# Kernel optimization log

Hardware: AMD Instinct MI355X
Metric: run time of the kernel (lower is better)

## Reference

```python
import jax, jax.numpy as jnp
import numpy as np


def haar_level(x):
    """One 2D Haar (periodization-equivalent for even sizes) DWT on [B,K,C,H,W].
    Returns [B,4K,C,H/2,W/2] with per-parent band order (LL, Hx, Hy, Hxy),
    matching the tree's append order yl, yh0, yh1, yh2."""
    B, K, C, H, W = x.shape
    x = x.reshape(B, K, C, H // 2, 2, W // 2, 2)
    a = x[:, :, :, :, 0, :, 0]
    b = x[:, :, :, :, 0, :, 1]
    c = x[:, :, :, :, 1, :, 0]
    d = x[:, :, :, :, 1, :, 1]
    ll = (a + b + c + d) * 0.5
    h1 = (a - b + c - d) * 0.5   # high along width
    h2 = (a + b - c - d) * 0.5   # high along height
    h3 = (a - b - c + d) * 0.5   # diagonal
    out = jnp.stack([ll, h1, h2, h3], axis=2)  # [B,K,4,C,H/2,W/2]
    return out.reshape(B, 4 * K, C, H // 2, W // 2)


def conv2d(x, w, b, stride, pad):
    y = jax.lax.conv_general_dilated(
        x, w, window_strides=(stride, stride),
        padding=[(pad, pad), (pad, pad)],
        dimension_numbers=('NCHW', 'OIHW', 'NCHW'))
    return y + b[None, :, None, None]


def setup_inputs() -> dict:
    key = jax.random.key(0)
    ks = jax.random.split(key, 9)
    s = 0.05
    return {
        'x':        jax.random.normal(ks[0], (64, 3, 224, 224), dtype=jnp.float32),
        'w_s1':     jax.random.normal(ks[1], (192, 3, 7, 7), dtype=jnp.float32) * s,
        'b_s1':     jax.random.normal(ks[2], (192,), dtype=jnp.float32) * s,
        'w_s2':     jax.random.normal(ks[3], (192, 192, 7, 7), dtype=jnp.float32) * s,
        'b_s2':     jax.random.normal(ks[4], (192,), dtype=jnp.float32) * s,
        'w_p':      jax.random.normal(ks[5], (768, 960, 3, 3), dtype=jnp.float32) * s,
        'b_p':      jax.random.normal(ks[6], (768,), dtype=jnp.float32) * s,
        'cls_token': jax.random.normal(ks[7], (1, 1, 768), dtype=jnp.float32),
        'positions': jax.random.normal(ks[8], (50, 768), dtype=jnp.float32),
    }


def reference(x, w_s1, b_s1, w_s2, b_s2, w_p, b_p, cls_token, positions):
    B = x.shape[0]
    # ---- 4-level full Haar wavelet packet tree (vectorized over subbands) ----
    t = x[:, None]                      # [B,1,3,224,224]
    for _ in range(4):
        t = haar_level(t)               # -> [B,256,3,14,14]
    wav = t.reshape(B, 256 * 3, 14, 14)  # [B,768,14,14] (tree concat order)
    # ---- spatial branch: two strided 7x7 convs (224 -> 56 -> 14) ----
    sp = conv2d(x, w_s1, b_s1, stride=4, pad=3)
    sp = conv2d(sp, w_s2, b_s2, stride=4, pad=3)   # [B,192,14,14]
    feat = jnp.concatenate([wav, sp], axis=1)      # [B,960,14,14]
    # ---- patch projection conv 3x3 s2 -> 7x7, flatten to tokens ----
    y = conv2d(feat, w_p, b_p, stride=2, pad=1)    # [B,768,7,7]
    y = y.reshape(B, 768, 49).transpose(0, 2, 1)   # [B,49,768]
    cls = jnp.broadcast_to(cls_token, (B, 1, 768))
    y = jnp.concatenate([cls, y], axis=1) + positions  # [B,50,768]
    return y
```

## Files before the change

### kernel.cpp

```cpp
#include <hip/hip_runtime.h>
#include <stdint.h>

typedef __attribute__((ext_vector_type(8))) short short8;
typedef __attribute__((ext_vector_type(4))) float floatx4;

__device__ inline unsigned short f2bf(float f){
  union { float fv; unsigned int u; } v; v.fv = f;
  unsigned int u = v.u;
  unsigned int r = ((u >> 16) & 1u) + 0x7FFFu;
  return (unsigned short)((u + r) >> 16);
}

__device__ __forceinline__ void async16(const void* g, void* l){
  __builtin_amdgcn_global_load_lds(
      (const __attribute__((address_space(1))) unsigned int*)g,
      (__attribute__((address_space(3))) unsigned int*)l, 16, 0, 0);
}

#define PBAR(N) do {                                              \
    asm volatile("s_waitcnt vmcnt(" #N ")" ::: "memory");          \
    __builtin_amdgcn_s_barrier();                                  \
    asm volatile("" ::: "memory");                                 \
  } while (0)

__global__ void prep_w1(const float* __restrict__ w, unsigned short* __restrict__ w1p){
  int i = blockIdx.x*256 + threadIdx.x;
  if (i >= 192*192) return;
  int k = i % 192, o = i / 192;
  int cc = k >> 3, kx = k & 7;
  unsigned short v = 0;
  if (cc < 21 && kx < 7){
    int c = cc / 7, ky = cc % 7;
    v = f2bf(w[(o*3 + c)*49 + ky*7 + kx]);
  }
  w1p[i] = v;
}
__global__ void prep_w2(const float* __restrict__ w, unsigned short* __restrict__ w2p){
  int i = blockIdx.x*256 + threadIdx.x;
  if (i >= 192*9408) return;
  int k = i % 9408, o = i / 9408;
  int g = k / 192, c = k % 192;
  int ky = g / 7, kx = g % 7;
  w2p[i] = f2bf(w[((o*192 + c)*7 + ky)*7 + kx]);
}
__global__ void prep_w3(const float* __restrict__ w, unsigned short* __restrict__ w3p){
  int i = blockIdx.x*256 + threadIdx.x;
  if (i >= 768*8640) return;
  int k = i % 8640, o = i / 8640;
  int g = k / 960, c = k % 960;
  int ky = g / 3, kx = g % 3;
  w3p[i] = f2bf(w[((o*960 + c)*3 + ky)*3 + kx]);
}
__global__ void prep_zp(unsigned int* __restrict__ zp){
  zp[threadIdx.x] = 0u;
}
__global__ void zero_f32(float* __restrict__ p, int n){
  int i = blockIdx.x*256 + threadIdx.x;
  if (i < n) p[i] = 0.f;
}

__global__ void pad_x8(const float* __restrict__ x, unsigned short* __restrict__ xh2){
  int idx = blockIdx.x*256 + threadIdx.x;
  int ox = idx % 56; int t = idx / 56;
  int iy = t % 230;  t /= 230;
  int row = iy - 3;
  short8 o = (short8){0,0,0,0,0,0,0,0};
  if ((unsigned)row < 224u){
    const float* src = x + ((size_t)t*224 + row)*224;
    int cbase = 4*ox - 3;
    #pragma unroll
    for (int kx = 0; kx < 8; kx++){
      int col = cbase + kx;
      if ((unsigned)col < 224u) o[kx] = (short)f2bf(src[col]);
    }
  }
  *(short8*)(xh2 + (size_t)idx*8) = o;
}

__global__ void wavelet_kernel(const float* __restrict__ x, unsigned short* __restrict__ feat){
  int blk = blockIdx.x;
  int j = blk % 14; blk /= 14;
  int i = blk % 14; blk /= 14;
  int c = blk % 3;  int b = blk / 3;
  int t = threadIdx.x;
  int u = t >> 4, v = t & 15;
  float val = x[((size_t)(b*3 + c)*224 + (i*16 + u))*224 + (j*16 + v)];
  #pragma unroll
  for (int bit = 1; bit < 64; bit <<= 1){
    float p = __shfl_xor(val, bit);
    val = (t & bit) ? (p - val) : (val + p);
  }
  __shared__ float s[256];
  #pragma unroll
  for (int bit = 64; bit < 256; bit <<= 1){
    s[t] = val; __syncthreads();
    float p = s[t ^ bit]; __syncthreads();
    val = (t & bit) ? (p - val) : (val + p);
  }
  s[t] = val; __syncthreads();
  int k = t;
  int d1 = (k>>6)&3, d2 = (k>>4)&3, d3 = (k>>2)&3, d4 = k&3;
  int mr = (d1>>1) | ((d2>>1)<<1) | ((d3>>1)<<2) | ((d4>>1)<<3);
  int mc = (d1&1)  | ((d2&1)<<1)  | ((d3&1)<<2)  | ((d4&1)<<3);
  float outv = s[mr*16 + mc] * 0.0625f;
  feat[((size_t)((b*14 + i)*14 + j))*960 + (k*3 + c)] = f2bf(outv);
}

__global__ __launch_bounds__(256) void conv1_gemm(const unsigned short* __restrict__ xh2,
                                                  const unsigned short* __restrict__ w1p,
                                                  const float* __restrict__ b1,
                                                  unsigned short* __restrict__ sp1){
  __shared__ unsigned short As[2][128*64], Bs[2][64*64];
  int m0 = blockIdx.x*128, n0 = blockIdx.y*64;
  int tid = threadIdx.x, wave = tid >> 6, lane = tid & 63;
  int l16 = lane & 15, quad = lane >> 4;
  int wy = wave >> 1, wx = wave & 1;
  int r8 = lane >> 3, kb = (lane & 7) ^ r8;

  int Abase[4];
  #pragma unroll
  for (int j = 0; j < 4; j++){
    int row = wave*32 + j*8 + r8;
    int m = m0 + row;
    int ox = m % 56; int t = m / 56; int oy = t % 56; int b = t / 56;
    Abase[j] = (b*690 + 4*oy)*448 + ox*8;
  }
  const unsigned short* pB0 = w1p + (n0 + wave*16 + r8)*192 + kb*8;
  const unsigned short* pB1 = pB0 + 8*192;

  int sw = l16 & 7;
  int xo0 = ((quad    ) ^ sw)*8;
  int xo1 = ((quad + 4) ^ sw)*8;
  int aoff[4];
  #pragma unroll
  for (int mt = 0; mt < 4; mt++) aoff[mt] = (wy*64 + mt*16 + l16)*64;
  int boff0 = (wx*32 + l16)*64, boff1 = boff0 + 16*64;

  floatx4 acc[4][2];
  #pragma unroll
  for (int mt = 0; mt < 4; mt++)
    #pragma unroll
    for (int nt = 0; nt < 2; nt++) acc[mt][nt] = (floatx4){0.f,0.f,0.f,0.f};

  auto stage = [&](int i, int buf){
    int cc = i*8 + kb;
    int c = (cc*147) >> 10;
    int ky = cc - 7*c;
    int koff = (c*230 + ky)*448;
    #pragma unroll
    for (int j = 0; j < 4; j++)
      async16(xh2 + Abase[j] + koff, (void*)&As[buf][(wave*32 + j*8)*64]);
    async16(pB0 + i*64, (void*)&Bs[buf][(wave*16    )*64]);
    async16(pB1 + i*64, (void*)&Bs[buf][(wave*16 + 8)*64]);
  };

  stage(0, 0);
  __syncthreads();
  #pragma unroll
  for (int i = 0; i < 3; i++){
    int buf = i & 1;
    if (i < 2) stage(i+1, buf ^ 1);
    #pragma unroll
    for (int ks = 0; ks < 2; ks++){
      int xo = ks ? xo1 : xo0;
      short8 b0 = *(const short8*)&Bs[buf][boff0 + xo];
      short8 b1 = *(const short8*)&Bs[buf][boff1 + xo];
      #pragma unroll
      for (int mt = 0; mt < 4; mt++){
        short8 a = *(const short8*)&As[buf][aoff[mt] + xo];
        acc[mt][0] = __builtin_amdgcn_mfma_f32_16x16x32_bf16(a, b0, acc[mt][0], 0, 0, 0);
        acc[mt][1] = __builtin_amdgcn_mfma_f32_16x16x32_bf16(a, b1, acc[mt][1], 0, 0, 0);
      }
    }
    __syncthreads();
  }

  #pragma unroll
  for (int mt = 0; mt < 4; mt++){
    #pragma unroll
    for (int rg = 0; rg < 4; rg++){
      int row = wy*64 + mt*16 + quad*4 + rg;
      size_t ob = (size_t)(m0 + row)*192;
      #pragma unroll
      for (int nt = 0; nt < 2; nt++){
        int nn = n0 + wx*32 + nt*16 + l16;
        sp1[ob + nn] = f2bf(acc[mt][nt][rg] + b1[nn]);
      }
    }
  }
}

template<int MODE>
__global__ __launch_bounds__(256, 4) void conv_ks(const unsigned short* __restrict__ Ain,
                                                  const unsigned short* __restrict__ Bt,
                                                  const unsigned short* __restrict__ zp,
                                                  float* __restrict__ pout){
  constexpr int OH  = (MODE==2) ? 14 : 7;
  constexpr int OW  = OH;
  constexpr int IH  = (MODE==2) ? 56 : 14;
  constexpr int IW  = IH;
  constexpr int Cin = (MODE==2) ? 192 : 960;
  constexpr int KW  = (MODE==2) ? 7 : 3;
  constexpr int S   = (MODE==2) ? 4 : 2;
  constexpr int P   = (MODE==2) ? 3 : 1;
  constexpr int K   = (MODE==2) ? 9408 : 8640;
  constexpr int NBODY = K/32;
  constexpr int KSEG  = 4;
  constexpr int MTI = (MODE==2) ? 98 : 25;
  constexpr int NTI = (MODE==2) ? 3 : 12;
  constexpr int GRP = 8*NTI;
  constexpr int PERSEG = (MODE==2) ? 13*GRP : 4*GRP;
  constexpr int M   = (MODE==2) ? 12544 : 3136;
  constexpr int NF  = (MODE==2) ? 192 : 768;

  int id = blockIdx.x;
  int kseg = id / PERSEG; int rem = id % PERSEG;
  int g = rem / GRP, r2 = rem % GRP;
  int mtile = g*8 + (r2 & 7);
  if (mtile >= MTI) return;
  int ntile = r2 >> 3;
  int m0 = mtile*128, n0 = ntile*64;

  int bs = (NBODY*kseg)/KSEG, be = (NBODY*(kseg+1))/KSEG;
  int NB = be - bs;
  int k0 = bs*32;

  __shared__ unsigned short As[3][4096], Bs[3][2048];

  int tid = threadIdx.x, wv = tid >> 6, lane = tid & 63;
  int l16 = lane & 15, quad = lane >> 4;
  int wy = wv >> 1, wx = wv & 1;

  int rl = lane >> 2;
  int go = ((lane & 3) ^ ((lane >> 3) & 3))*8;

  int iyb[2], ixb[2], abase[2];
  #pragma unroll
  for (int j = 0; j < 2; j++){
    int r = (wv + j*4)*16 + rl;
    int m = m0 + r; if (MODE == 3 && m > M-1) m = M-1;
    int ox = m % OW; int t = m / OW; int oy = t % OH; int bb = t / OH;
    iyb[j] = S*oy - P; ixb[j] = S*ox - P;
    abase[j] = ((bb*IH + iyb[j])*IW + ixb[j])*Cin + go;
  }
  const unsigned short* pB = Bt + (size_t)(n0 + wv*16 + rl)*K + k0 + go;

  int c0 = k0 % Cin;
  int gk = k0 / Cin;
  int ky = gk / KW, kx = gk % KW;
  int k0n = 0;

  int xo = (quad ^ ((l16 >> 1) & 3))*8;

  floatx4 acc[4][2];
  #pragma unroll
  for (int mt = 0; mt < 4; mt++)
    #pragma unroll
    for (int nt = 0; nt < 2; nt++) acc[mt][nt] = (floatx4){0.f,0.f,0.f,0.f};

  auto stage = [&](int buf){
    int koff = (ky*IW + kx)*Cin + c0;
    #pragma unroll
    for (int j = 0; j < 2; j++){
      int iy = iyb[j] + ky, ix = ixb[j] + kx;
      const unsigned short* pa = ((unsigned)iy < (unsigned)IH && (unsigned)ix < (unsigned)IW)
                                 ? (Ain + abase[j] + koff) : zp;
      async16(pa, (void*)&As[buf][(wv + j*4)*512]);
    }
    async16(pB + k0n, (void*)&Bs[buf][wv*512]);
    k0n += 32;
    c0 += 32;
    if (c0 == Cin){ c0 = 0; kx++; if (kx == KW){ kx = 0; ky++; } }
  };

  auto compute = [&](int buf){
    short8 b0 = *(const short8*)&Bs[buf][(wx*32      + l16)*32 + xo];
    short8 b1 = *(const short8*)&Bs[buf][(wx*32 + 16 + l16)*32 + xo];
    short8 a0 = *(const short8*)&As[buf][(wy*64       + l16)*32 + xo];
    short8 a1 = *(const short8*)&As[buf][(wy*64 + 16  + l16)*32 + xo];
    short8 a2 = *(const short8*)&As[buf][(wy*64 + 32  + l16)*32 + xo];
    short8 a3 = *(const short8*)&As[buf][(wy*64 + 48  + l16)*32 + xo];
    acc[0][0] = __builtin_amdgcn_mfma_f32_16x16x32_bf16(a0, b0, acc[0][0], 0, 0, 0);
    acc[0][1] = __builtin_amdgcn_mfma_f32_16x16x32_bf16(a0, b1, acc[0][1], 0, 0, 0);
    acc[1][0] = __builtin_amdgcn_mfma_f32_16x16x32_bf16(a1, b0, acc[1][0], 0, 0, 0);
    acc[1][1] = __builtin_amdgcn_mfma_f32_16x16x32_bf16(a1, b1, acc[1][1], 0, 0, 0);
    acc[2][0] = __builtin_amdgcn_mfma_f32_16x16x32_bf16(a2, b0, acc[2][0], 0, 0, 0);
    acc[2][1] = __builtin_amdgcn_mfma_f32_16x16x32_bf16(a2, b1, acc[2][1], 0, 0, 0);
    acc[3][0] = __builtin_amdgcn_mfma_f32_16x16x32_bf16(a3, b0, acc[3][0], 0, 0, 0);
    acc[3][1] = __builtin_amdgcn_mfma_f32_16x16x32_bf16(a3, b1, acc[3][1], 0, 0, 0);
  };

  stage(0); stage(1);
  int bc = 0;
  for (int i = 0; i < NB - 2; i++){
    PBAR(3);
    int bn = bc + 2; if (bn >= 3) bn -= 3;
    stage(bn);
    compute(bc);
    bc = (bc == 2) ? 0 : bc + 1;
  }
  PBAR(3);
  compute(bc);
  bc = (bc == 2) ? 0 : bc + 1;
  PBAR(0);
  compute(bc);

  #pragma unroll
  for (int mt = 0; mt < 4; mt++){
    #pragma unroll
    for (int rg = 0; rg < 4; rg++){
      int row = wy*64 + mt*16 + quad*4 + rg;
      int mm = m0 + row;
      if (MODE == 3 && mm >= M) continue;
      #pragma unroll
      for (int nt = 0; nt < 2; nt++){
        int nn = n0 + wx*32 + nt*16 + l16;
        atomicAdd(&pout[(size_t)mm*NF + nn], acc[mt][nt][rg]);
      }
    }
  }
}

__global__ void comb2(const float* __restrict__ pc, const float* __restrict__ bias,
                      unsigned short* __restrict__ feat){
  int i = blockIdx.x*256 + threadIdx.x;
  int n = i % 192, m = i / 192;
  feat[(size_t)m*960 + 768 + n] = f2bf(pc[i] + bias[n]);
}
__global__ void comb3(const float* __restrict__ pc, const float* __restrict__ bias,
                      const float* __restrict__ pos, float* __restrict__ out){
  int i = blockIdx.x*256 + threadIdx.x;
  int n = i % 768, m = i / 768;
  int b2 = m / 49, tt = m - b2*49;
  float v = pc[(size_t)m*768 + n] + bias[n] + pos[(size_t)(1 + tt)*768 + n];
  out[((size_t)(m + b2 + 1))*768 + n] = v;
}

__global__ void cls_kernel(const float* __restrict__ cls, const float* __restrict__ pos,
                           float* __restrict__ out){
  int i = blockIdx.x*256 + threadIdx.x;
  if (i >= 64*768) return;
  int e = i % 768, b = i / 768;
  out[(size_t)(b*50)*768 + e] = cls[e] + pos[e];
}

extern "C" void kernel_launch(void* const* d_in, const int* in_sizes, int n_in,
                              void* d_out, int out_size, void* d_ws, size_t ws_size,
                              hipStream_t stream){
  (void)in_sizes; (void)n_in; (void)out_size;
  const float* x    = (const float*)d_in[0];
  const float* w_s1 = (const float*)d_in[1];
  const float* b_s1 = (const float*)d_in[2];
  const float* w_s2 = (const float*)d_in[3];
  const float* b_s2 = (const float*)d_in[4];
  const float* w_p  = (const float*)d_in[5];
  const float* b_p  = (const float*)d_in[6];
  const float* cls  = (const float*)d_in[7];
  const float* pos  = (const float*)d_in[8];
  float* out = (float*)d_out;

  char* ws = (char*)d_ws;
  if (ws_size < 118235136u) return;
  unsigned short* w1p  = (unsigned short*)(ws + 0);
  unsigned short* sp1  = (unsigned short*)(ws + 131072);
  unsigned short* zp   = (unsigned short*)(ws + 77201408u);
  unsigned short* w2p  = (unsigned short*)(ws + 77266944u);
  unsigned short* w3p  = (unsigned short*)(ws + 80879616u);
  unsigned short* feat = (unsigned short*)(ws + 94150656u);
  unsigned short* xh2  = (unsigned short*)(ws + 77266944u);
  float* pc2 = (float*)(ws + 80879616u);
  float* pc3 = (float*)(ws + 131072);

  prep_w1<<<(192*192 + 255)/256, 256, 0, stream>>>(w_s1, w1p);
  pad_x8<<<64*3*230*56/256, 256, 0, stream>>>(x, xh2);
  conv1_gemm<<<dim3(1568, 3), 256, 0, stream>>>(xh2, w1p, b_s1, sp1);
  prep_w2<<<(192*9408 + 255)/256, 256, 0, stream>>>(w_s2, w2p);
  prep_zp<<<1, 64, 0, stream>>>((unsigned int*)zp);
  wavelet_kernel<<<64*3*14*14, 256, 0, stream>>>(x, feat);

  zero_f32<<<9408, 256, 0, stream>>>(pc2, 12544*192);
  conv_ks<2><<<1248, 256, 0, stream>>>(sp1, w2p, zp, pc2);
  comb2<<<9408, 256, 0, stream>>>(pc2, b_s2, feat);

  prep_w3<<<(768*8640 + 255)/256, 256, 0, stream>>>(w_p, w3p);
  zero_f32<<<9600, 256, 0, stream>>>(pc3, 3200*768);
  conv_ks<3><<<1536, 256, 0, stream>>>(feat, w3p, zp, pc3);
  comb3<<<9408, 256, 0, stream>>>(pc3, b_p, pos, out);
  cls_kernel<<<(64*768 + 255)/256, 256, 0, stream>>>(cls, pos, out);
}
```

Before: 482.8 us.

## Widen conv K-step to 64 and halve split-K segments

```diff
diff --git a/kernel.cpp b/kernel.cpp
--- a/kernel.cpp
+++ b/kernel.cpp
@@ -191,10 +191,10 @@
 }
 
 template<int MODE>
-__global__ __launch_bounds__(256, 4) void conv_ks(const unsigned short* __restrict__ Ain,
-                                                  const unsigned short* __restrict__ Bt,
-                                                  const unsigned short* __restrict__ zp,
-                                                  float* __restrict__ pout){
+__global__ __launch_bounds__(256) void conv_ks2(const unsigned short* __restrict__ Ain,
+                                                const unsigned short* __restrict__ Bt,
+                                                const unsigned short* __restrict__ zp,
+                                                float* __restrict__ pout){
   constexpr int OH  = (MODE==2) ? 14 : 7;
   constexpr int OW  = OH;
   constexpr int IH  = (MODE==2) ? 56 : 14;
@@ -204,8 +204,8 @@
   constexpr int S   = (MODE==2) ? 4 : 2;
   constexpr int P   = (MODE==2) ? 3 : 1;
   constexpr int K   = (MODE==2) ? 9408 : 8640;
-  constexpr int NBODY = K/32;
-  constexpr int KSEG  = 4;
+  constexpr int NBODY = K/64;
+  constexpr int KSEG  = 2;
   constexpr int MTI = (MODE==2) ? 98 : 25;
   constexpr int NTI = (MODE==2) ? 3 : 12;
   constexpr int GRP = 8*NTI;
@@ -223,34 +223,39 @@
 
   int bs = (NBODY*kseg)/KSEG, be = (NBODY*(kseg+1))/KSEG;
   int NB = be - bs;
-  int k0 = bs*32;
-
-  __shared__ unsigned short As[3][4096], Bs[3][2048];
-
-  int tid = threadIdx.x, wv = tid >> 6, lane = tid & 63;
+  int ksg0 = bs*64;
+
+  __shared__ unsigned short As[3][128*64], Bs[3][64*64];
+
+  int tid = threadIdx.x, wave = tid >> 6, lane = tid & 63;
   int l16 = lane & 15, quad = lane >> 4;
-  int wy = wv >> 1, wx = wv & 1;
-
-  int rl = lane >> 2;
-  int go = ((lane & 3) ^ ((lane >> 3) & 3))*8;
-
-  int iyb[2], ixb[2], abase[2];
-  #pragma unroll
-  for (int j = 0; j < 2; j++){
-    int r = (wv + j*4)*16 + rl;
-    int m = m0 + r; if (MODE == 3 && m > M-1) m = M-1;
+  int wy = wave >> 1, wx = wave & 1;
+  int r8 = lane >> 3, kb = (lane & 7) ^ r8;
+  int sw = l16 & 7;
+
+  int abase[4], iyb[4], ixb[4];
+  #pragma unroll
+  for (int j = 0; j < 4; j++){
+    int row = wave*32 + j*8 + r8;
+    int m = m0 + row; if (MODE == 3 && m > M-1) m = M-1;
     int ox = m % OW; int t = m / OW; int oy = t % OH; int bb = t / OH;
     iyb[j] = S*oy - P; ixb[j] = S*ox - P;
-    abase[j] = ((bb*IH + iyb[j])*IW + ixb[j])*Cin + go;
-  }
-  const unsigned short* pB = Bt + (size_t)(n0 + wv*16 + rl)*K + k0 + go;
-
-  int c0 = k0 % Cin;
-  int gk = k0 / Cin;
+    abase[j] = ((bb*IH + iyb[j])*IW + ixb[j])*Cin + kb*8;
+  }
+  const unsigned short* pB0 = Bt + (size_t)(n0 + wave*16 + r8)*K + ksg0 + kb*8;
+  const unsigned short* pB1 = pB0 + (size_t)8*K;
+
+  int c0 = ksg0 % Cin;
+  int gk = ksg0 / Cin;
   int ky = gk / KW, kx = gk % KW;
   int k0n = 0;
 
-  int xo = (quad ^ ((l16 >> 1) & 3))*8;
+  int xo0 = ((quad    ) ^ sw)*8;
+  int xo1 = ((quad + 4) ^ sw)*8;
+  int aoff[4];
+  #pragma unroll
+  for (int mt = 0; mt < 4; mt++) aoff[mt] = (wy*64 + mt*16 + l16)*64;
+  int boff0 = (wx*32 + l16)*64, boff1 = boff0 + 16*64;
 
   floatx4 acc[4][2];
   #pragma unroll
@@ -261,45 +266,44 @@
   auto stage = [&](int buf){
     int koff = (ky*IW + kx)*Cin + c0;
     #pragma unroll
-    for (int j = 0; j < 2; j++){
+    for (int j = 0; j < 4; j++){
       int iy = iyb[j] + ky, ix = ixb[j] + kx;
       const unsigned short* pa = ((unsigned)iy < (unsigned)IH && (unsigned)ix < (unsigned)IW)
                                  ? (Ain + abase[j] + koff) : zp;
-      async16(pa, (void*)&As[buf][(wv + j*4)*512]);
-    }
-    async16(pB + k0n, (void*)&Bs[buf][wv*512]);
-    k0n += 32;
-    c0 += 32;
+      async16(pa, (void*)&As[buf][(wave*32 + j*8)*64]);
+    }
+    async16(pB0 + k0n, (void*)&Bs[buf][(wave*16    )*64]);
+    async16(pB1 + k0n, (void*)&Bs[buf][(wave*16 + 8)*64]);
+    k0n += 64;
+    c0 += 64;
     if (c0 == Cin){ c0 = 0; kx++; if (kx == KW){ kx = 0; ky++; } }
   };
 
   auto compute = [&](int buf){
-    short8 b0 = *(const short8*)&Bs[buf][(wx*32      + l16)*32 + xo];
-    short8 b1 = *(const short8*)&Bs[buf][(wx*32 + 16 + l16)*32 + xo];
-    short8 a0 = *(const short8*)&As[buf][(wy*64       + l16)*32 + xo];
-    short8 a1 = *(const short8*)&As[buf][(wy*64 + 16  + l16)*32 + xo];
-    short8 a2 = *(const short8*)&As[buf][(wy*64 + 32  + l16)*32 + xo];
-    short8 a3 = *(const short8*)&As[buf][(wy*64 + 48  + l16)*32 + xo];
-    acc[0][0] = __builtin_amdgcn_mfma_f32_16x16x32_bf16(a0, b0, acc[0][0], 0, 0, 0);
-    acc[0][1] = __builtin_amdgcn_mfma_f32_16x16x32_bf16(a0, b1, acc[0][1], 0, 0, 0);
-    acc[1][0] = __builtin_amdgcn_mfma_f32_16x16x32_bf16(a1, b0, acc[1][0], 0, 0, 0);
-    acc[1][1] = __builtin_amdgcn_mfma_f32_16x16x32_bf16(a1, b1, acc[1][1], 0, 0, 0);
-    acc[2][0] = __builtin_amdgcn_mfma_f32_16x16x32_bf16(a2, b0, acc[2][0], 0, 0, 0);
-    acc[2][1] = __builtin_amdgcn_mfma_f32_16x16x32_bf16(a2, b1, acc[2][1], 0, 0, 0);
-    acc[3][0] = __builtin_amdgcn_mfma_f32_16x16x32_bf16(a3, b0, acc[3][0], 0, 0, 0);
-    acc[3][1] = __builtin_amdgcn_mfma_f32_16x16x32_bf16(a3, b1, acc[3][1], 0, 0, 0);
+    #pragma unroll
+    for (int ks = 0; ks < 2; ks++){
+      int xo = ks ? xo1 : xo0;
+      short8 b0 = *(const short8*)&Bs[buf][boff0 + xo];
+      short8 b1 = *(const short8*)&Bs[buf][boff1 + xo];
+      #pragma unroll
+      for (int mt = 0; mt < 4; mt++){
+        short8 a = *(const short8*)&As[buf][aoff[mt] + xo];
+        acc[mt][0] = __builtin_amdgcn_mfma_f32_16x16x32_bf16(a, b0, acc[mt][0], 0, 0, 0);
+        acc[mt][1] = __builtin_amdgcn_mfma_f32_16x16x32_bf16(a, b1, acc[mt][1], 0, 0, 0);
+      }
+    }
   };
 
   stage(0); stage(1);
   int bc = 0;
   for (int i = 0; i < NB - 2; i++){
-    PBAR(3);
+    PBAR(6);
     int bn = bc + 2; if (bn >= 3) bn -= 3;
     stage(bn);
     compute(bc);
     bc = (bc == 2) ? 0 : bc + 1;
   }
-  PBAR(3);
+  PBAR(6);
   compute(bc);
   bc = (bc == 2) ? 0 : bc + 1;
   PBAR(0);
@@ -379,12 +383,12 @@
   wavelet_kernel<<<64*3*14*14, 256, 0, stream>>>(x, feat);
 
   zero_f32<<<9408, 256, 0, stream>>>(pc2, 12544*192);
-  conv_ks<2><<<1248, 256, 0, stream>>>(sp1, w2p, zp, pc2);
+  conv_ks2<2><<<624, 256, 0, stream>>>(sp1, w2p, zp, pc2);
   comb2<<<9408, 256, 0, stream>>>(pc2, b_s2, feat);
 
   prep_w3<<<(768*8640 + 255)/256, 256, 0, stream>>>(w_p, w3p);
   zero_f32<<<9600, 256, 0, stream>>>(pc3, 3200*768);
-  conv_ks<3><<<1536, 256, 0, stream>>>(feat, w3p, zp, pc3);
+  conv_ks2<3><<<768, 256, 0, stream>>>(feat, w3p, zp, pc3);
   comb3<<<9408, 256, 0, stream>>>(pc3, b_p, pos, out);
   cls_kernel<<<(64*768 + 255)/256, 256, 0, stream>>>(cls, pos, out);
 }
```

New measurement: 502.0 us. 1.04x slower.
